# Kernel optimization log

Hardware: AMD Instinct MI355X
Metric: run time of the kernel (lower is better)

The kernel has to match this reference:

```python
import jax, jax.numpy as jnp
import numpy as np

B, N, E, D, P = 128, 50000, 300000, 256, 8


def setup_inputs() -> dict:
    key = jax.random.key(0)
    ks = jax.random.split(key, 13)
    scale = 1.0 / np.sqrt(D)  # keep uniform-init logits numerically sane
    return {
        "instruction_batch": jax.random.normal(ks[0], (B, D), jnp.float32),
        "distribution": jax.random.uniform(ks[1], (N,), jnp.float32),
        "node_prop_similarities": jax.random.uniform(ks[2], (B, P), jnp.float32),
        "relation_similarity": jax.random.uniform(ks[3], (B,), jnp.float32),
        "node_attrs": jax.random.normal(ks[4], (N, D), jnp.float32),
        "edge_attrs": jax.random.normal(ks[5], (E, D), jnp.float32),
        "W_node_props": jax.random.uniform(ks[6], (P, D, D), jnp.float32) * scale,
        "W_edge": jax.random.uniform(ks[7], (D, D), jnp.float32) * scale,
        "w_node_score": jax.random.uniform(ks[8], (D,), jnp.float32) * scale,
        "w_rel_score": jax.random.uniform(ks[9], (D,), jnp.float32) * scale,
        "node_indices": jnp.sort(jax.random.randint(ks[10], (N,), 0, B)),
        "edge_batch_indices": jax.random.randint(ks[11], (E,), 0, B),
        "edge_indices": jax.random.randint(ks[12], (2, E), 0, N),
    }


def _segment_softmax(logits, seg, num_segments):
    # softmax over all entries sharing the same segment (= per-graph softmax)
    m = jax.ops.segment_max(logits, seg, num_segments=num_segments)
    e = jnp.exp(logits - m[seg])
    s = jax.ops.segment_sum(e, seg, num_segments=num_segments)
    return e / s[seg]


def reference(instruction_batch, distribution, node_prop_similarities,
              relation_similarity, node_attrs, edge_attrs,
              W_node_props, W_edge, w_node_score, w_rel_score,
              node_indices, edge_batch_indices, edge_indices):
    num_graphs = instruction_batch.shape[0]

    # node_scores[n,d] = elu( sum_p sim[n,p] * instr[n,d] * (W_p @ attr_n)[d] )
    sim_n = node_prop_similarities[node_indices]          # [N, P]
    instr_n = instruction_batch[node_indices]             # [N, D]
    wa = jnp.einsum("pde,ne->npd", W_node_props, node_attrs)  # [N, P, D]
    node_scores = jax.nn.elu(
        jnp.einsum("np,nd,npd->nd", sim_n, instr_n, wa))   # [N, D]

    # edge_scores[e,d] = elu( instr[batch(e),d] * (W_edge @ edge_attr_e)[d] )
    edge_scores = jax.nn.elu(
        instruction_batch[edge_batch_indices] * (edge_attrs @ W_edge.T))  # [E, D]

    # per-graph (sparse) softmax over node state logits
    state_logits = node_scores @ w_node_score              # [N]
    next_states = _segment_softmax(state_logits, node_indices, num_graphs)

    # scatter: aggregate weighted edge messages at destination nodes
    src, dst = edge_indices[0], edge_indices[1]
    msgs = distribution[src, None] * edge_scores           # [E, D]
    agg = jnp.zeros_like(node_scores).at[dst].add(msgs)    # [N, D]
    rel_logits = agg @ w_rel_score                         # [N]
    next_relations = _segment_softmax(rel_logits, node_indices, num_graphs)

    r = relation_similarity[node_indices]                  # [N]
    return r * next_relations + (1.0 - r) * next_states
```

## Files before the change

### kernel.cpp

```cpp
#include <hip/hip_runtime.h>

#define NB 128
#define NN 50000
#define NE 300000
#define ND 256
#define NP 8

typedef __attribute__((ext_vector_type(4))) float f32x4;
typedef __attribute__((ext_vector_type(8))) short s16x8;

__device__ __forceinline__ unsigned short bf16rtn(float f) {
    unsigned int u = __float_as_uint(f);
    unsigned int r = (u + 0x7fffu + ((u >> 16) & 1u)) >> 16;
    return (unsigned short)r;
}

__device__ __forceinline__ s16x8 pack8(f32x4 a, f32x4 b) {
    s16x8 v;
    v[0] = (short)bf16rtn(a[0]); v[1] = (short)bf16rtn(a[1]);
    v[2] = (short)bf16rtn(a[2]); v[3] = (short)bf16rtn(a[3]);
    v[4] = (short)bf16rtn(b[0]); v[5] = (short)bf16rtn(b[1]);
    v[6] = (short)bf16rtn(b[2]); v[7] = (short)bf16rtn(b[3]);
    return v;
}

__device__ __forceinline__ float eluf(float x) {
    return x > 0.f ? x : __expf(x) - 1.f;
}

__device__ __forceinline__ float rowsum16(float x) {
    int t;
    t = __builtin_amdgcn_update_dpp(0, __float_as_int(x), 0x121, 0xf, 0xf, true);
    x += __int_as_float(t);
    t = __builtin_amdgcn_update_dpp(0, __float_as_int(x), 0x122, 0xf, 0xf, true);
    x += __int_as_float(t);
    t = __builtin_amdgcn_update_dpp(0, __float_as_int(x), 0x124, 0xf, 0xf, true);
    x += __int_as_float(t);
    t = __builtin_amdgcn_update_dpp(0, __float_as_int(x), 0x128, 0xf, 0xf, true);
    x += __int_as_float(t);
    return x;
}

__device__ __forceinline__ void stage_W(char* Wl, const unsigned short* Wsrc,
                                        int tid, int nthr) {
    for (int i = tid; i < 8192; i += nthr) {
        int cg = i >> 9;
        int kk = (i >> 6) & 7;
        int ln = i & 63;
        const unsigned short* src =
            Wsrc + (size_t)(cg * 16 + (ln & 15)) * ND + kk * 32 + (ln >> 4) * 8;
        *(s16x8*)(Wl + i * 16) = *(const s16x8*)src;
    }
}

__global__ void k_starts(const int* __restrict__ idx, int* __restrict__ starts,
                         float* __restrict__ rel_logits) {
    int n = blockIdx.x * blockDim.x + threadIdx.x;
    if (n >= NN) return;
    rel_logits[n] = 0.f;
    int cur = idx[n];
    int prev = (n == 0) ? -1 : idx[n - 1];
    for (int b2 = prev + 1; b2 <= cur; ++b2) starts[b2] = n;
    if (n == NN - 1)
        for (int b2 = cur + 1; b2 <= NB; ++b2) starts[b2] = NN;
}

__global__ void k_dsc(const int* __restrict__ eidx, const float* __restrict__ dist,
                      float* __restrict__ dscg) {
    int e = blockIdx.x * blockDim.x + threadIdx.x;
    if (e < NE) dscg[e] = dist[eidx[e]];
}

__global__ void k_wedge_bf16(const float* __restrict__ w, unsigned short* __restrict__ o) {
    int i = (blockIdx.x * 256 + threadIdx.x) * 4;
    f32x4 v = *(const f32x4*)(w + i);
    o[i + 0] = bf16rtn(v[0]); o[i + 1] = bf16rtn(v[1]);
    o[i + 2] = bf16rtn(v[2]); o[i + 3] = bf16rtn(v[3]);
}

__global__ __launch_bounds__(256) void k_weff(
    const float* __restrict__ sim, const float* __restrict__ Wp,
    unsigned short* __restrict__ Weff)
{
    int chunk = blockIdx.x * 256 + threadIdx.x;
    int off = chunk * 8;
    float wp[NP][8];
#pragma unroll
    for (int p = 0; p < NP; ++p) {
        const float* src = Wp + (size_t)p * ND * ND + off;
        f32x4 w0 = *(const f32x4*)src;
        f32x4 w1 = *(const f32x4*)(src + 4);
        wp[p][0] = w0[0]; wp[p][1] = w0[1]; wp[p][2] = w0[2]; wp[p][3] = w0[3];
        wp[p][4] = w1[0]; wp[p][5] = w1[1]; wp[p][6] = w1[2]; wp[p][7] = w1[3];
    }
    int b0 = blockIdx.y * 16;
    for (int bb = 0; bb < 16; ++bb) {
        int b = b0 + bb;
        float g[8] = {0.f, 0.f, 0.f, 0.f, 0.f, 0.f, 0.f, 0.f};
#pragma unroll
        for (int p = 0; p < NP; ++p) {
            float s = sim[b * NP + p];
#pragma unroll
            for (int j = 0; j < 8; ++j) g[j] += s * wp[p][j];
        }
        s16x8 v;
#pragma unroll
        for (int j = 0; j < 8; ++j) v[j] = (short)bf16rtn(g[j]);
        *(s16x8*)(Weff + (size_t)b * ND * ND + off) = v;
    }
}

__global__ __launch_bounds__(1024, 4) void k_edges(
    const float* __restrict__ instr, const float* __restrict__ dscg,
    const float* __restrict__ eattrs, const unsigned short* __restrict__ Wbf,
    const float* __restrict__ wrs, const int* __restrict__ ebidx,
    const int* __restrict__ eidx, float* __restrict__ rel_logits)
{
    __shared__ char Wl[131072];

    int tid = threadIdx.x;
    int lane = tid & 63;
    int wave = tid >> 6;
    int l15 = lane & 15;
    int q = lane >> 4;

    stage_W(Wl, Wbf, tid, 1024);
    __syncthreads();

    int gw = blockIdx.x * 16 + wave;
    const int NT = NE / 16;
    for (int t = gw; t < NT; t += 4096) {
        int e0 = t * 16;
        const float* ib0 = instr + (size_t)ebidx[e0 + 4 * q + 0] * ND + l15;
        const float* ib1 = instr + (size_t)ebidx[e0 + 4 * q + 1] * ND + l15;
        const float* ib2 = instr + (size_t)ebidx[e0 + 4 * q + 2] * ND + l15;
        const float* ib3 = instr + (size_t)ebidx[e0 + 4 * q + 3] * ND + l15;

        const float* arow = eattrs + (size_t)(e0 + l15) * ND + q * 8;
        s16x8 afr[8];
#pragma unroll
        for (int kk = 0; kk < 8; ++kk) {
            f32x4 a0 = *(const f32x4*)(arow + kk * 32);
            f32x4 a1 = *(const f32x4*)(arow + kk * 32 + 4);
            afr[kk] = pack8(a0, a1);
        }

        float p0 = 0.f, p1 = 0.f, p2 = 0.f, p3 = 0.f;
#pragma unroll 1
        for (int cg = 0; cg < 16; ++cg) {
            f32x4 acc = {0.f, 0.f, 0.f, 0.f};
            const char* fb = Wl + cg * 8192 + lane * 16;
#pragma unroll
            for (int kk = 0; kk < 8; ++kk) {
                s16x8 bf = *(const s16x8*)(fb + kk * 1024);
                acc = __builtin_amdgcn_mfma_f32_16x16x32_bf16(afr[kk], bf, acc, 0, 0, 0);
            }
            float wvc = wrs[cg * 16 + l15];
            int c = cg * 16;
            p0 += wvc * eluf(ib0[c] * acc[0]);
            p1 += wvc * eluf(ib1[c] * acc[1]);
            p2 += wvc * eluf(ib2[c] * acc[2]);
            p3 += wvc * eluf(ib3[c] * acc[3]);
        }
        p0 = rowsum16(p0); p1 = rowsum16(p1);
        p2 = rowsum16(p2); p3 = rowsum16(p3);
        if (l15 == 0) {
            int e = e0 + 4 * q;
            atomicAdd(&rel_logits[eidx[NE + e + 0]], dscg[e + 0] * p0);
            atomicAdd(&rel_logits[eidx[NE + e + 1]], dscg[e + 1] * p1);
            atomicAdd(&rel_logits[eidx[NE + e + 2]], dscg[e + 2] * p2);
            atomicAdd(&rel_logits[eidx[NE + e + 3]], dscg[e + 3] * p3);
        }
    }
}

__global__ __launch_bounds__(1024, 4) void k_nodes(
    const float* __restrict__ instr, const unsigned short* __restrict__ Weff,
    const float* __restrict__ attrs, const float* __restrict__ wns,
    const int* __restrict__ starts, float* __restrict__ state_logits)
{
    __shared__ char Wl[131072];

    int b = blockIdx.x >> 1;
    int half = blockIdx.x & 1;
    int s0 = starts[b], s1 = starts[b + 1];
    int nt = (s1 - s0 + 15) >> 4;

    int tid = threadIdx.x;
    int lane = tid & 63;
    int wave = tid >> 6;
    int l15 = lane & 15;
    int q = lane >> 4;

    stage_W(Wl, Weff + (size_t)b * ND * ND, tid, 1024);
    __syncthreads();

    const float* irow = instr + (size_t)b * ND + l15;
    for (int t = half * 16 + wave; t < nt; t += 32) {
        int n0 = s0 + t * 16;
        int arn = n0 + l15;
        bool valid = arn < s1;
        const float* arow = attrs + (size_t)arn * ND + q * 8;
        s16x8 afr[8];
#pragma unroll
        for (int kk = 0; kk < 8; ++kk) {
            f32x4 a0 = {0.f, 0.f, 0.f, 0.f}, a1 = {0.f, 0.f, 0.f, 0.f};
            if (valid) {
                a0 = *(const f32x4*)(arow + kk * 32);
                a1 = *(const f32x4*)(arow + kk * 32 + 4);
            }
            afr[kk] = pack8(a0, a1);
        }

        float p0 = 0.f, p1 = 0.f, p2 = 0.f, p3 = 0.f;
#pragma unroll 1
        for (int cg = 0; cg < 16; ++cg) {
            f32x4 acc = {0.f, 0.f, 0.f, 0.f};
            const char* fb = Wl + cg * 8192 + lane * 16;
#pragma unroll
            for (int kk = 0; kk < 8; ++kk) {
                s16x8 bf = *(const s16x8*)(fb + kk * 1024);
                acc = __builtin_amdgcn_mfma_f32_16x16x32_bf16(afr[kk], bf, acc, 0, 0, 0);
            }
            int c = cg * 16;
            float ivc = irow[c];
            float wvc = wns[c + l15];
            p0 += wvc * eluf(ivc * acc[0]);
            p1 += wvc * eluf(ivc * acc[1]);
            p2 += wvc * eluf(ivc * acc[2]);
            p3 += wvc * eluf(ivc * acc[3]);
        }
        p0 = rowsum16(p0); p1 = rowsum16(p1);
        p2 = rowsum16(p2); p3 = rowsum16(p3);
        if (l15 == 0) {
            int n = n0 + 4 * q;
            if (n + 0 < s1) state_logits[n + 0] = p0;
            if (n + 1 < s1) state_logits[n + 1] = p1;
            if (n + 2 < s1) state_logits[n + 2] = p2;
            if (n + 3 < s1) state_logits[n + 3] = p3;
        }
    }
}

__global__ __launch_bounds__(256) void k_softmax_mix(
    const float* __restrict__ state_l, const float* __restrict__ rel_l,
    const int* __restrict__ starts, const float* __restrict__ relsim,
    float* __restrict__ out)
{
    __shared__ float wms[4], wmr[4], wss[4], wsr[4];
    int b = blockIdx.x;
    int s0 = starts[b], s1 = starts[b + 1];
    if (s1 <= s0) return;
    int tid = threadIdx.x, lane = tid & 63, wave = tid >> 6;

    float ms = -3.4e38f, mr = -3.4e38f;
    for (int n = s0 + tid; n < s1; n += 256) {
        ms = fmaxf(ms, state_l[n]);
        mr = fmaxf(mr, rel_l[n]);
    }
#pragma unroll
    for (int m = 1; m < 64; m <<= 1) {
        ms = fmaxf(ms, __shfl_xor(ms, m, 64));
        mr = fmaxf(mr, __shfl_xor(mr, m, 64));
    }
    if (lane == 0) { wms[wave] = ms; wmr[wave] = mr; }
    __syncthreads();
    ms = fmaxf(fmaxf(wms[0], wms[1]), fmaxf(wms[2], wms[3]));
    mr = fmaxf(fmaxf(wmr[0], wmr[1]), fmaxf(wmr[2], wmr[3]));

    float ss = 0.f, sr = 0.f;
    for (int n = s0 + tid; n < s1; n += 256) {
        ss += __expf(state_l[n] - ms);
        sr += __expf(rel_l[n] - mr);
    }
#pragma unroll
    for (int m = 1; m < 64; m <<= 1) {
        ss += __shfl_xor(ss, m, 64);
        sr += __shfl_xor(sr, m, 64);
    }
    if (lane == 0) { wss[wave] = ss; wsr[wave] = sr; }
    __syncthreads();
    ss = wss[0] + wss[1] + wss[2] + wss[3];
    sr = wsr[0] + wsr[1] + wsr[2] + wsr[3];

    float rb = relsim[b];
    float iss = 1.f / ss, isr = 1.f / sr;
    for (int n = s0 + tid; n < s1; n += 256) {
        out[n] = rb * __expf(rel_l[n] - mr) * isr
               + (1.f - rb) * __expf(state_l[n] - ms) * iss;
    }
}

extern "C" void kernel_launch(void* const* d_in, const int* in_sizes, int n_in,
                              void* d_out, int out_size, void* d_ws, size_t ws_size,
                              hipStream_t stream) {
    const float* instr  = (const float*)d_in[0];
    const float* dist   = (const float*)d_in[1];
    const float* sim    = (const float*)d_in[2];
    const float* relsim = (const float*)d_in[3];
    const float* nattr  = (const float*)d_in[4];
    const float* eattr  = (const float*)d_in[5];
    const float* Wp     = (const float*)d_in[6];
    const float* We     = (const float*)d_in[7];
    const float* wns    = (const float*)d_in[8];
    const float* wrs    = (const float*)d_in[9];
    const int* nidx     = (const int*)d_in[10];
    const int* ebidx    = (const int*)d_in[11];
    const int* eidx     = (const int*)d_in[12];
    float* out = (float*)d_out;

    char* ws = (char*)d_ws;
    float* rel_logits   = (float*)ws;
    float* state_logits = rel_logits + NN;
    int* starts         = (int*)(ws + 400000);
    unsigned short* Wbf = (unsigned short*)(ws + 400640);
    unsigned short* Weff= (unsigned short*)(ws + 532480);
    float* dscg         = (float*)(ws + 17309696);

    k_wedge_bf16<<<64, 256, 0, stream>>>(We, Wbf);
    k_weff<<<dim3(32, 8), 256, 0, stream>>>(sim, Wp, Weff);
    k_starts<<<(NN + 255) / 256, 256, 0, stream>>>(nidx, starts, rel_logits);
    k_dsc<<<(NE + 255) / 256, 256, 0, stream>>>(eidx, dist, dscg);
    k_edges<<<256, 1024, 0, stream>>>(instr, dscg, eattr, Wbf, wrs,
                                      ebidx, eidx, rel_logits);
    k_nodes<<<256, 1024, 0, stream>>>(instr, Weff, nattr, wns, starts,
                                      state_logits);
    k_softmax_mix<<<NB, 256, 0, stream>>>(state_logits, rel_logits, starts,
                                          relsim, out);
}
```

Before: 157.2 us.

## Split edge kernel output columns across block pairs to halve LDS weight tile

The edge kernel now launches 512 blocks of 512 threads, and each block pair splits the 256 output columns in half. Each block stages only a 64KB half of the bf16 W_edge into LDS, which allows more resident blocks per CU and cuts the per-block staging cost. In exchange every edge-attribute row is read and converted to bf16 twice (once per half), and each edge gets two atomic adds to rel_logits instead of one. Per-wave MFMA work per tile is halved.

```diff
diff --git a/kernel.cpp b/kernel.cpp
--- a/kernel.cpp
+++ b/kernel.cpp
@@ -42,13 +42,14 @@
 }
 
 __device__ __forceinline__ void stage_W(char* Wl, const unsigned short* Wsrc,
-                                        int tid, int nthr) {
-    for (int i = tid; i < 8192; i += nthr) {
+                                        int cg0, int ncg, int tid, int nthr) {
+    int total = ncg * 512;
+    for (int i = tid; i < total; i += nthr) {
         int cg = i >> 9;
         int kk = (i >> 6) & 7;
         int ln = i & 63;
         const unsigned short* src =
-            Wsrc + (size_t)(cg * 16 + (ln & 15)) * ND + kk * 32 + (ln >> 4) * 8;
+            Wsrc + (size_t)((cg0 + cg) * 16 + (ln & 15)) * ND + kk * 32 + (ln >> 4) * 8;
         *(s16x8*)(Wl + i * 16) = *(const s16x8*)src;
     }
 }
@@ -110,31 +111,36 @@
     }
 }
 
-__global__ __launch_bounds__(1024, 4) void k_edges(
+__global__ __launch_bounds__(512, 4) void k_edges(
     const float* __restrict__ instr, const float* __restrict__ dscg,
     const float* __restrict__ eattrs, const unsigned short* __restrict__ Wbf,
     const float* __restrict__ wrs, const int* __restrict__ ebidx,
     const int* __restrict__ eidx, float* __restrict__ rel_logits)
 {
-    __shared__ char Wl[131072];
+    __shared__ char Wl[65536];
 
     int tid = threadIdx.x;
     int lane = tid & 63;
     int wave = tid >> 6;
     int l15 = lane & 15;
     int q = lane >> 4;
-
-    stage_W(Wl, Wbf, tid, 1024);
+    int half = blockIdx.x & 1;
+    int co = half * 128;
+
+    stage_W(Wl, Wbf, half * 8, 8, tid, 512);
     __syncthreads();
 
-    int gw = blockIdx.x * 16 + wave;
+    int gw = (blockIdx.x >> 1) * 8 + wave;
     const int NT = NE / 16;
-    for (int t = gw; t < NT; t += 4096) {
+    for (int t = gw; t < NT; t += 2048) {
         int e0 = t * 16;
-        const float* ib0 = instr + (size_t)ebidx[e0 + 4 * q + 0] * ND + l15;
-        const float* ib1 = instr + (size_t)ebidx[e0 + 4 * q + 1] * ND + l15;
-        const float* ib2 = instr + (size_t)ebidx[e0 + 4 * q + 2] * ND + l15;
-        const float* ib3 = instr + (size_t)ebidx[e0 + 4 * q + 3] * ND + l15;
+        int e4 = e0 + 4 * q;
+        int eb0 = ebidx[e4 + 0], eb1 = ebidx[e4 + 1];
+        int eb2 = ebidx[e4 + 2], eb3 = ebidx[e4 + 3];
+        const float* ib0 = instr + (size_t)eb0 * ND + co + l15;
+        const float* ib1 = instr + (size_t)eb1 * ND + co + l15;
+        const float* ib2 = instr + (size_t)eb2 * ND + co + l15;
+        const float* ib3 = instr + (size_t)eb3 * ND + co + l15;
 
         const float* arow = eattrs + (size_t)(e0 + l15) * ND + q * 8;
         s16x8 afr[8];
@@ -147,7 +153,7 @@
 
         float p0 = 0.f, p1 = 0.f, p2 = 0.f, p3 = 0.f;
 #pragma unroll 1
-        for (int cg = 0; cg < 16; ++cg) {
+        for (int cg = 0; cg < 8; ++cg) {
             f32x4 acc = {0.f, 0.f, 0.f, 0.f};
             const char* fb = Wl + cg * 8192 + lane * 16;
 #pragma unroll
@@ -155,8 +161,8 @@
                 s16x8 bf = *(const s16x8*)(fb + kk * 1024);
                 acc = __builtin_amdgcn_mfma_f32_16x16x32_bf16(afr[kk], bf, acc, 0, 0, 0);
             }
-            float wvc = wrs[cg * 16 + l15];
             int c = cg * 16;
+            float wvc = wrs[co + c + l15];
             p0 += wvc * eluf(ib0[c] * acc[0]);
             p1 += wvc * eluf(ib1[c] * acc[1]);
             p2 += wvc * eluf(ib2[c] * acc[2]);
@@ -165,11 +171,10 @@
         p0 = rowsum16(p0); p1 = rowsum16(p1);
         p2 = rowsum16(p2); p3 = rowsum16(p3);
         if (l15 == 0) {
-            int e = e0 + 4 * q;
-            atomicAdd(&rel_logits[eidx[NE + e + 0]], dscg[e + 0] * p0);
-            atomicAdd(&rel_logits[eidx[NE + e + 1]], dscg[e + 1] * p1);
-            atomicAdd(&rel_logits[eidx[NE + e + 2]], dscg[e + 2] * p2);
-            atomicAdd(&rel_logits[eidx[NE + e + 3]], dscg[e + 3] * p3);
+            atomicAdd(&rel_logits[eidx[NE + e4 + 0]], dscg[e4 + 0] * p0);
+            atomicAdd(&rel_logits[eidx[NE + e4 + 1]], dscg[e4 + 1] * p1);
+            atomicAdd(&rel_logits[eidx[NE + e4 + 2]], dscg[e4 + 2] * p2);
+            atomicAdd(&rel_logits[eidx[NE + e4 + 3]], dscg[e4 + 3] * p3);
         }
     }
 }
@@ -192,7 +197,7 @@
     int l15 = lane & 15;
     int q = lane >> 4;
 
-    stage_W(Wl, Weff + (size_t)b * ND * ND, tid, 1024);
+    stage_W(Wl, Weff + (size_t)b * ND * ND, 0, 16, tid, 1024);
     __syncthreads();
 
     const float* irow = instr + (size_t)b * ND + l15;
@@ -321,8 +326,8 @@
     k_weff<<<dim3(32, 8), 256, 0, stream>>>(sim, Wp, Weff);
     k_starts<<<(NN + 255) / 256, 256, 0, stream>>>(nidx, starts, rel_logits);
     k_dsc<<<(NE + 255) / 256, 256, 0, stream>>>(eidx, dist, dscg);
-    k_edges<<<256, 1024, 0, stream>>>(instr, dscg, eattr, Wbf, wrs,
-                                      ebidx, eidx, rel_logits);
+    k_edges<<<512, 512, 0, stream>>>(instr, dscg, eattr, Wbf, wrs,
+                                     ebidx, eidx, rel_logits);
     k_nodes<<<256, 1024, 0, stream>>>(instr, Weff, nattr, wns, starts,
                                       state_logits);
     k_softmax_mix<<<NB, 256, 0, stream>>>(state_logits, rel_logits, starts,
```

Result: slower. 179.6 us (+14.2%).
